# Optimization experiments

Hardware: AMD Instinct MI355X
Metric: run time of the kernel (lower is better)

Reference implementation:

```python
import jax, jax.numpy as jnp
import numpy as np

K = 20  # neighbors per point

def binq(x):
    # XNOR-Net style sign binarization with straight-through estimator
    return x + jax.lax.stop_gradient(jnp.sign(x) - x)

def knn_idx(x, k):
    # x: (B, C, N) -> (B, N, k) indices of k nearest neighbors (incl. self)
    xt = jnp.swapaxes(x, 1, 2)                      # (B, N, C)
    inner = jnp.einsum('bnc,bmc->bnm', xt, xt)
    sq = jnp.sum(xt * xt, axis=-1)                  # (B, N)
    neg_d = 2.0 * inner - sq[:, :, None] - sq[:, None, :]
    _, idx = jax.lax.top_k(neg_d, k)
    return idx

def graph_feature(x, k):
    # DGCNN edge features: (B, C, N) -> (B, 2C, N, k), plus edge index
    idx = knn_idx(x, k)
    xt = jnp.swapaxes(x, 1, 2)                      # (B, N, C)
    nb = jax.vmap(lambda t, i: t[i])(xt, idx)       # (B, N, k, C)
    ctr = jnp.broadcast_to(xt[:, :, None, :], nb.shape)
    feat = jnp.concatenate([nb - ctr, ctr], axis=-1)  # (B, N, k, 2C)
    return jnp.transpose(feat, (0, 3, 1, 2)), idx

def conv2d_block(x, W, a, s, b, p, bin_in):
    # binary-weight 1x1 conv (XNOR-Net++ channel rescale a) + eval-BN affine (s,b) + PReLU(p)
    xb = binq(x) if bin_in else x
    y = jnp.einsum('bcnk,oc->bonk', xb, binq(W))
    y = y * (a * s)[None, :, None, None] + b[None, :, None, None]
    return jnp.where(y > 0, y, p[None, :, None, None] * y)

def conv1d_block(x, W, a, s, b, p):
    y = jnp.einsum('bcn,oc->bon', binq(x), binq(W))
    y = y * (a * s)[None, :, None] + b[None, :, None]
    return jnp.where(y > 0, y, p[None, :, None] * y)

def lin_block(x, W, a, s, b, p):
    y = (binq(x) @ binq(W).T) * (a * s) + b
    return jnp.where(y > 0, y, p * y)

def forward(x0, w1, a1, s1, b1, p1, w2, a2, s2, b2, p2, w3, a3, s3, b3, p3,
            w4, a4, s4, b4, p4, w5, a5, s5, b5, p5,
            wl1, al1, sl1, bl1, pl1, wl2, al2, sl2, bl2, pl2, wl3, sl3, bl3):
    f, _ = graph_feature(x0, K)
    x1 = conv2d_block(f, w1, a1, s1, b1, p1, False).max(axis=-1)   # (B,64,N)
    f, _ = graph_feature(x1, K)
    x2 = conv2d_block(f, w2, a2, s2, b2, p2, True).max(axis=-1)    # (B,64,N)
    f, _ = graph_feature(x2, K)
    x3 = conv2d_block(f, w3, a3, s3, b3, p3, True).max(axis=-1)    # (B,128,N)
    f, _ = graph_feature(x3, K)
    x4 = conv2d_block(f, w4, a4, s4, b4, p4, True).max(axis=-1)    # (B,256,N)
    x = jnp.concatenate([x1, x2, x3, x4], axis=1)                  # (B,512,N)
    x = conv1d_block(x, w5, a5, s5, b5, p5)                        # (B,1024,N)
    x = jnp.concatenate([x.max(axis=-1), x.mean(axis=-1)], axis=1)  # (B,2048)
    x = lin_block(x, wl1, al1, sl1, bl1, pl1)                      # (B,512)
    x = lin_block(x, wl2, al2, sl2, bl2, pl2)                      # (B,256)
    return (x @ wl3.T) * sl3 + bl3                                 # (B,40) logits

def setup_inputs():
    key = jax.random.key(0)
    ks = iter(jax.random.split(key, 16))
    B, N = 16, 1024
    d = {'x0': jax.random.normal(next(ks), (B, 3, N), jnp.float32)}
    def block(name, co, ci, has_prelu=True, has_alpha=True):
        d['w' + name] = jax.random.normal(next(ks), (co, ci), jnp.float32) * 0.05
        if has_alpha:
            d['a' + name] = jnp.ones((co,), jnp.float32)
        d['s' + name] = jnp.ones((co,), jnp.float32)
        d['b' + name] = jnp.zeros((co,), jnp.float32)
        if has_prelu:
            d['p' + name] = jnp.full((co,), 0.25, jnp.float32)
    block('1', 64, 6)
    block('2', 64, 128)
    block('3', 128, 128)
    block('4', 256, 256)
    block('5', 1024, 512)
    block('l1', 512, 2048)
    block('l2', 256, 512)
    block('l3', 40, 256, has_prelu=False, has_alpha=False)
    return d

def reference(x0, w1, a1, s1, b1, p1, w2, a2, s2, b2, p2, w3, a3, s3, b3, p3,
              w4, a4, s4, b4, p4, w5, a5, s5, b5, p5,
              wl1, al1, sl1, bl1, pl1, wl2, al2, sl2, bl2, pl2, wl3, sl3, bl3):
    return forward(x0, w1, a1, s1, b1, p1, w2, a2, s2, b2, p2, w3, a3, s3, b3, p3,
                   w4, a4, s4, b4, p4, w5, a5, s5, b5, p5,
                   wl1, al1, sl1, bl1, pl1, wl2, al2, sl2, bl2, pl2, wl3, sl3, bl3)
```

## Files before the change

kernel.cpp:

```cpp
#include <hip/hip_runtime.h>
#include <math.h>

#define B 16
#define N 1024
#define KNB 20

typedef unsigned int u32;
typedef unsigned long long u64;

__device__ __forceinline__ float sgnf(float v) {
    return (v > 0.f) ? 1.f : ((v < 0.f) ? -1.f : 0.f);
}

__global__ __launch_bounds__(256) void sentinel_kernel(float* __restrict__ out, int n, float v) {
    int i = blockIdx.x * blockDim.x + threadIdx.x;
    if (i < n) out[i] = v;
}


template <int C>
__global__ __launch_bounds__(256) void sq_np_kernel(const float* __restrict__ x, int Ctot, int c0,
                                                    float* __restrict__ sq) {
    int i = blockIdx.x * blockDim.x + threadIdx.x;
    if (i >= B * N) return;
    int b = i >> 10, n = i & (N - 1);
    const float* xb = x + ((size_t)b * Ctot + c0) * N + n;
    float res;
    if (C < 8) {
        float v0 = xb[0];
        res = __fmul_rn(v0, v0);
        for (int c = 1; c < C; ++c) {
            float v = xb[(size_t)c * N];
            res = __fadd_rn(res, __fmul_rn(v, v));
        }
    } else {
        float r[8];
#pragma unroll
        for (int j = 0; j < 8; ++j) {
            float v = xb[(size_t)j * N];
            r[j] = __fmul_rn(v, v);
        }
        for (int c = 8; c < C; c += 8) {
#pragma unroll
            for (int j = 0; j < 8; ++j) {
                float v = xb[(size_t)(c + j) * N];
                r[j] = __fadd_rn(r[j], __fmul_rn(v, v));
            }
        }
        res = __fadd_rn(__fadd_rn(__fadd_rn(r[0], r[1]), __fadd_rn(r[2], r[3])),
                        __fadd_rn(__fadd_rn(r[4], r[5]), __fadd_rn(r[6], r[7])));
    }
    sq[i] = res;
}

template <int C>
__global__ __launch_bounds__(128) void knn_radix4_kernel(const float* __restrict__ x, int Ctot,
                                                         int c0, const float* __restrict__ sq,
                                                         int* __restrict__ idxout) {
    const int b = blockIdx.y;
    const int tid = threadIdx.x, wave = tid >> 6, lane = tid & 63;
    const int nbase = blockIdx.x * 8;
    __shared__ float xn[C][8];
    const float* xb = x + ((size_t)b * Ctot + c0) * N;
    for (int t = tid; t < 8 * C; t += 128) {
        int pt = t & 7, c = t >> 3;
        xn[c][pt] = xb[(size_t)c * N + nbase + pt];
    }
    __syncthreads();
    float acc[4][16];
#pragma unroll
    for (int p = 0; p < 4; ++p)
#pragma unroll
        for (int j = 0; j < 16; ++j) acc[p][j] = 0.f;
    const int w4 = wave * 4;
    for (int c = 0; c < C; ++c) {
        const float* row = xb + (size_t)c * N + lane;
        float xv0 = xn[c][w4 + 0], xv1 = xn[c][w4 + 1];
        float xv2 = xn[c][w4 + 2], xv3 = xn[c][w4 + 3];
#pragma unroll
        for (int j = 0; j < 16; ++j) {
            float rv = row[j * 64];
            acc[0][j] = __fadd_rn(acc[0][j], __fmul_rn(xv0, rv));
            acc[1][j] = __fadd_rn(acc[1][j], __fmul_rn(xv1, rv));
            acc[2][j] = __fadd_rn(acc[2][j], __fmul_rn(xv2, rv));
            acc[3][j] = __fadd_rn(acc[3][j], __fmul_rn(xv3, rv));
        }
    }
    float sqm[16];
#pragma unroll
    for (int j = 0; j < 16; ++j) sqm[j] = sq[b * N + j * 64 + lane];
    const u64 ltmask = (1ull << lane) - 1ull;
#pragma unroll
    for (int p = 0; p < 4; ++p) {
        const int n = nbase + w4 + p;
        const float sqn = sq[b * N + n];
        u32 key[16];
#pragma unroll
        for (int j = 0; j < 16; ++j) {
            float d = __fsub_rn(__fsub_rn(__fmul_rn(2.f, acc[p][j]), sqn), sqm[j]);
            u32 bits = __float_as_uint(d);
            if ((bits << 1) == 0) bits = 0;
            key[j] = (bits & 0x80000000u) ? ~bits : (bits | 0x80000000u);
        }
        u32 T = 0;
        for (int bpos = 31; bpos >= 0; --bpos) {
            u32 cand = T | (1u << bpos);
            int cnt = 0;
#pragma unroll
            for (int j = 0; j < 16; ++j) cnt += __popcll(__ballot(key[j] >= cand));
            if (cnt >= KNB) T = cand;
        }
        int* out = idxout + ((size_t)b * N + n) * KNB;
        int base = 0;
#pragma unroll
        for (int j = 0; j < 16; ++j) {
            u64 m = __ballot(key[j] > T);
            if (key[j] > T) out[base + __popcll(m & ltmask)] = j * 64 + lane;
            base += __popcll(m);
        }
        const int R = KNB - base;
        int eqb = 0;
#pragma unroll
        for (int j = 0; j < 16; ++j) {
            u64 m = __ballot(key[j] == T);
            int r = eqb + __popcll(m & ltmask);
            if (key[j] == T && r < R) out[base + r] = j * 64 + lane;
            eqb += __popcll(m);
        }
    }
}


__global__ __launch_bounds__(256) void transpose3_kernel(const float* __restrict__ x,
                                                         float* __restrict__ xT) {
    int i = blockIdx.x * blockDim.x + threadIdx.x;
    if (i >= B * N) return;
    int b = i >> 10, n = i & (N - 1);
    xT[(size_t)i * 3 + 0] = x[((size_t)b * 3 + 0) * N + n];
    xT[(size_t)i * 3 + 1] = x[((size_t)b * 3 + 1) * N + n];
    xT[(size_t)i * 3 + 2] = x[((size_t)b * 3 + 2) * N + n];
}


__global__ __launch_bounds__(256) void transpose_rm2cm_kernel(const float* __restrict__ yR, int CO,
                                                              float* __restrict__ xcat, int c0) {
    const int nb = blockIdx.x * 64, cb = blockIdx.y * 64, b = blockIdx.z;
    const int tid = threadIdx.x;
    __shared__ float t[64][65];
    for (int i = tid; i < 64 * 64; i += 256) {
        int nn = i >> 6, cc = i & 63;
        t[nn][cc] = yR[((size_t)(b * N + nb + nn)) * CO + cb + cc];
    }
    __syncthreads();
    for (int i = tid; i < 64 * 64; i += 256) {
        int cc = i >> 6, nn = i & 63;
        xcat[((size_t)b * 256 + c0 + cb + cc) * N + nb + nn] = t[nn][cc];
    }
}


template <int C, int COUT>
__global__ __launch_bounds__(COUT) void edgeconv1_kernel(
    const float* __restrict__ xR, const int* __restrict__ idx, const float* __restrict__ W,
    const float* __restrict__ aa, const float* __restrict__ ssc, const float* __restrict__ bbi,
    const float* __restrict__ pp, float* __restrict__ yR, u32* __restrict__ xss,
    u32* __restrict__ xnzs, int woff) {
    const int b = blockIdx.y, n = blockIdx.x, tid = threadIdx.x;
    __shared__ float ctr_raw[C];
    __shared__ float df[C][KNB];
    __shared__ int ids[KNB];
    const float* xb = xR + (size_t)b * N * C;
    if (tid < KNB) ids[tid] = idx[((size_t)b * N + n) * KNB + tid];
    if (tid < C) ctr_raw[tid] = xb[(size_t)n * C + tid];
    __syncthreads();
    for (int t = tid; t < C * KNB; t += COUT) {
        int c = t / KNB, k = t - c * KNB;
        df[c][k] = __fsub_rn(xb[(size_t)ids[k] * C + c], ctr_raw[c]);
    }
    __syncthreads();
    const int o = tid;
    const float* wrow = W + (size_t)o * (2 * C);
    const float as = __fmul_rn(aa[o], ssc[o]);
    const float bo = bbi[o], po = pp[o];
    float best = -3.4e38f;
    float wd[C], wc[C];
    for (int c = 0; c < C; ++c) { wd[c] = sgnf(wrow[c]); wc[c] = sgnf(wrow[C + c]); }
    for (int k = 0; k < KNB; ++k) {
        float acc = 0.f;
        for (int c = 0; c < C; ++c) acc = __fadd_rn(acc, __fmul_rn(df[c][k], wd[c]));
        for (int c = 0; c < C; ++c) acc = __fadd_rn(acc, __fmul_rn(ctr_raw[c], wc[c]));
        float y = __fadd_rn(__fmul_rn(acc, as), bo);
        y = y > 0.f ? y : __fmul_rn(po, y);
        best = fmaxf(best, y);
    }
    yR[((size_t)b * N + n) * COUT + o] = best;
    u64 bs = __ballot(best < 0.f);
    u64 bnz = __ballot(best != 0.f);
    if ((tid & 63) == 0) {
        int w = woff + (tid >> 5);
        xss[(size_t)(b * 16 + w) * N + n] = (u32)bs;
        xss[(size_t)(b * 16 + w + 1) * N + n] = (u32)(bs >> 32);
        xnzs[(size_t)(b * 16 + w) * N + n] = (u32)bnz;
        xnzs[(size_t)(b * 16 + w + 1) * N + n] = (u32)(bnz >> 32);
    }
}


__global__ __launch_bounds__(256) void pack_rows_kernel(const float* __restrict__ src, int rows,
                                                        int cols, u32* __restrict__ s,
                                                        u32* __restrict__ nz) {
    int i = blockIdx.x * blockDim.x + threadIdx.x;
    int wpr = cols >> 5;
    if (i >= rows * wpr) return;
    int r = i / wpr, w = i - r * wpr;
    const float* p = src + (size_t)r * cols + (size_t)w * 32;
    u32 sb = 0, nb = 0;
    for (int j = 0; j < 32; ++j) {
        float v = p[j];
        if (v < 0.f) sb |= (1u << j);
        if (v != 0.f) nb |= (1u << j);
    }
    s[i] = sb;
    nz[i] = nb;
}


template <int C, int COUT, bool WRITEF>
__global__ __launch_bounds__(COUT) void edgeconv_bin2_kernel(
    const float* __restrict__ xR, const int* __restrict__ idx, const u32* __restrict__ wsm,
    const u32* __restrict__ wnzm, const float* __restrict__ aa, const float* __restrict__ ssc,
    const float* __restrict__ bbi, const float* __restrict__ pp, float* __restrict__ yR,
    u32* __restrict__ xss, u32* __restrict__ xnzs, int woff) {
    constexpr int W = C / 32;
    const int b = blockIdx.y, n = blockIdx.x, tid = threadIdx.x;
    __shared__ float ctr_raw[C];
    __shared__ int ids[KNB];
    __shared__ u32 ctr_s[W], ctr_nz[W];
    __shared__ u32 dfs[KNB][W], dfnz[KNB][W];
    const float* xb = xR + (size_t)b * N * C;
    if (tid < KNB) ids[tid] = idx[((size_t)b * N + n) * KNB + tid];
    if (tid < C) {
        float v = xb[(size_t)n * C + tid];
        ctr_raw[tid] = v;
        u64 bs = __ballot(v < 0.f);
        u64 bnz = __ballot(v != 0.f);
        if ((tid & 63) == 0) {
            int wb = tid >> 5;
            ctr_s[wb] = (u32)bs;       ctr_s[wb + 1] = (u32)(bs >> 32);
            ctr_nz[wb] = (u32)bnz;     ctr_nz[wb + 1] = (u32)(bnz >> 32);
        }
    }
    __syncthreads();
    for (int t = tid; t < KNB * C; t += COUT) {
        int k = t / C, c = t - k * C;
        float v = __fsub_rn(xb[(size_t)ids[k] * C + c], ctr_raw[c]);
        u64 bs = __ballot(v < 0.f);
        u64 bnz = __ballot(v != 0.f);
        if ((c & 63) == 0) {
            int wb = c >> 5;
            dfs[k][wb] = (u32)bs;      dfs[k][wb + 1] = (u32)(bs >> 32);
            dfnz[k][wb] = (u32)bnz;    dfnz[k][wb + 1] = (u32)(bnz >> 32);
        }
    }
    __syncthreads();
    const int o = tid;
    const u32* wsrow = wsm + (size_t)o * 2 * W;
    const u32* wnzrow = wnzm + (size_t)o * 2 * W;
    u32 wds[W], wdnz[W], wcs[W], wcnz[W];
#pragma unroll
    for (int w = 0; w < W; ++w) {
        wds[w] = wsrow[w];      wcs[w] = wsrow[W + w];
        wdnz[w] = wnzrow[w];    wcnz[w] = wnzrow[W + w];
    }
    int cdot = 0;
#pragma unroll
    for (int w = 0; w < W; ++w) {
        u32 nzb = ctr_nz[w] & wcnz[w];
        u32 neg = (ctr_s[w] ^ wcs[w]) & nzb;
        cdot += __popc(nzb) - 2 * __popc(neg);
    }
    const float as = __fmul_rn(aa[o], ssc[o]);
    const float bo = bbi[o], po = pp[o];
    float best = -3.4e38f;
    for (int k = 0; k < KNB; ++k) {
        int dot = cdot;
#pragma unroll
        for (int w = 0; w < W; ++w) {
            u32 nzb = dfnz[k][w] & wdnz[w];
            u32 neg = (dfs[k][w] ^ wds[w]) & nzb;
            dot += __popc(nzb) - 2 * __popc(neg);
        }
        float y = __fadd_rn(__fmul_rn((float)dot, as), bo);
        y = y > 0.f ? y : __fmul_rn(po, y);
        best = fmaxf(best, y);
    }
    if (WRITEF) yR[((size_t)b * N + n) * COUT + o] = best;
    u64 bs = __ballot(best < 0.f);
    u64 bnz = __ballot(best != 0.f);
    if ((tid & 63) == 0) {
        int w = woff + (tid >> 5);
        xss[(size_t)(b * 16 + w) * N + n] = (u32)bs;
        xss[(size_t)(b * 16 + w + 1) * N + n] = (u32)(bs >> 32);
        xnzs[(size_t)(b * 16 + w) * N + n] = (u32)bnz;
        xnzs[(size_t)(b * 16 + w + 1) * N + n] = (u32)(bnz >> 32);
    }
}


__global__ __launch_bounds__(256) void conv1d_bin_pool_kernel(
    const u32* __restrict__ xs, const u32* __restrict__ xnz, const u32* __restrict__ w5s,
    const u32* __restrict__ w5nz, const float* __restrict__ aa, const float* __restrict__ ssc,
    const float* __restrict__ bbi, const float* __restrict__ pp, float* __restrict__ pmax,
    float* __restrict__ psum) {
    const int b = blockIdx.y;
    const int otile = blockIdx.x & 3;
    const int nq = blockIdx.x >> 2;
    const int tid = threadIdx.x;
    const int o = otile * 256 + tid;
    __shared__ u32 shs[64][21];
    __shared__ u32 shnz[64][21];
    u32 ws[16], wnz[16];
#pragma unroll
    for (int w = 0; w < 16; ++w) {
        ws[w] = w5s[(size_t)o * 16 + w];
        wnz[w] = w5nz[(size_t)o * 16 + w];
    }
    const int nbase = nq * 64;
    for (int t = tid; t < 16 * 64; t += 256) {
        int w = t >> 6, nl = t & 63;
        shs[nl][w] = xs[((size_t)b * 16 + w) * N + nbase + nl];
        shnz[nl][w] = xnz[((size_t)b * 16 + w) * N + nbase + nl];
    }
    __syncthreads();
    const float as = __fmul_rn(aa[o], ssc[o]);
    const float bo = bbi[o], po = pp[o];
    float m = -3.4e38f, sum = 0.f;
    for (int nl = 0; nl < 64; ++nl) {
        int dot = 0;
#pragma unroll
        for (int w = 0; w < 16; ++w) {
            u32 nzb = shnz[nl][w] & wnz[w];
            u32 neg = (shs[nl][w] ^ ws[w]) & nzb;
            dot += __popc(nzb) - 2 * __popc(neg);
        }
        float y = __fadd_rn(__fmul_rn((float)dot, as), bo);
        y = y > 0.f ? y : __fmul_rn(po, y);
        m = fmaxf(m, y);
        sum = __fadd_rn(sum, y);
    }
    pmax[((size_t)b * 1024 + o) * 16 + nq] = m;
    psum[((size_t)b * 1024 + o) * 16 + nq] = sum;
}

__global__ __launch_bounds__(256) void pool_reduce_kernel(const float* __restrict__ pmax,
                                                          const float* __restrict__ psum,
                                                          float* __restrict__ pooled) {
    int i = blockIdx.x * blockDim.x + threadIdx.x;
    if (i >= B * 1024) return;
    int b = i >> 10, o = i & 1023;
    const float* pm = pmax + (size_t)i * 16;
    const float* ps = psum + (size_t)i * 16;
    float m = -3.4e38f, s = 0.f;
    for (int t = 0; t < 16; ++t) { m = fmaxf(m, pm[t]); s = __fadd_rn(s, ps[t]); }
    pooled[(size_t)b * 2048 + o] = m;
    pooled[(size_t)b * 2048 + 1024 + o] = __fmul_rn(s, (1.f / 1024.f));
}

__global__ __launch_bounds__(256) void pack_pooled_kernel(const float* __restrict__ pooled,
                                                          u32* __restrict__ s,
                                                          u32* __restrict__ nz) {
    int i = blockIdx.x * blockDim.x + threadIdx.x;
    if (i >= B * 64) return;
    const float* p = pooled + (size_t)i * 32;
    u32 sb = 0, nb = 0;
    for (int j = 0; j < 32; ++j) {
        float v = p[j];
        if (v < 0.f) sb |= (1u << j);
        if (v != 0.f) nb |= (1u << j);
    }
    s[i] = sb;
    nz[i] = nb;
}


__global__ __launch_bounds__(256) void lin1_bin_kernel(
    const u32* __restrict__ xs, const u32* __restrict__ xnz, const u32* __restrict__ wls,
    const u32* __restrict__ wlnz, const float* __restrict__ aa, const float* __restrict__ ssc,
    const float* __restrict__ bbi, const float* __restrict__ pp, u32* __restrict__ l1s,
    u32* __restrict__ l1nz) {
    const int b = blockIdx.y, otile = blockIdx.x, tid = threadIdx.x;
    const int o = otile * 256 + tid;
    __shared__ u32 sxs[64], sxnz[64];
    if (tid < 64) { sxs[tid] = xs[b * 64 + tid]; sxnz[tid] = xnz[b * 64 + tid]; }
    __syncthreads();
    const u32* wsr = wls + (size_t)o * 64;
    const u32* wnzr = wlnz + (size_t)o * 64;
    int dot = 0;
#pragma unroll
    for (int w = 0; w < 64; ++w) {
        u32 nzb = sxnz[w] & wnzr[w];
        u32 neg = (sxs[w] ^ wsr[w]) & nzb;
        dot += __popc(nzb) - 2 * __popc(neg);
    }
    float y = __fadd_rn(__fmul_rn((float)dot, __fmul_rn(aa[o], ssc[o])), bbi[o]);
    y = y > 0.f ? y : __fmul_rn(pp[o], y);
    u64 bs = __ballot(y < 0.f);
    u64 bnz = __ballot(y != 0.f);
    if ((tid & 63) == 0) {
        int w = otile * 8 + (tid >> 5);
        l1s[b * 16 + w] = (u32)bs;       l1s[b * 16 + w + 1] = (u32)(bs >> 32);
        l1nz[b * 16 + w] = (u32)bnz;     l1nz[b * 16 + w + 1] = (u32)(bnz >> 32);
    }
}

__global__ __launch_bounds__(256) void lin2_bin_kernel(
    const u32* __restrict__ xs, const u32* __restrict__ xnz, const u32* __restrict__ wls,
    const u32* __restrict__ wlnz, const float* __restrict__ aa, const float* __restrict__ ssc,
    const float* __restrict__ bbi, const float* __restrict__ pp, float* __restrict__ out) {
    const int b = blockIdx.x, o = threadIdx.x;
    __shared__ u32 sxs[16], sxnz[16];
    if (o < 16) { sxs[o] = xs[b * 16 + o]; sxnz[o] = xnz[b * 16 + o]; }
    __syncthreads();
    const u32* wsr = wls + (size_t)o * 16;
    const u32* wnzr = wlnz + (size_t)o * 16;
    int dot = 0;
#pragma unroll
    for (int w = 0; w < 16; ++w) {
        u32 nzb = sxnz[w] & wnzr[w];
        u32 neg = (sxs[w] ^ wsr[w]) & nzb;
        dot += __popc(nzb) - 2 * __popc(neg);
    }
    float y = __fadd_rn(__fmul_rn((float)dot, __fmul_rn(aa[o], ssc[o])), bbi[o]);
    out[b * 256 + o] = y > 0.f ? y : __fmul_rn(pp[o], y);
}

__global__ __launch_bounds__(64) void lin3_kernel(const float* __restrict__ xin,
                                                  const float* __restrict__ W,
                                                  const float* __restrict__ ssc,
                                                  const float* __restrict__ bbi,
                                                  float* __restrict__ out) {
    int b = blockIdx.x, j = threadIdx.x;
    if (j >= 40) return;
    const float* wrow = W + j * 256;
    const float* xb = xin + b * 256;
    double acc = 0.0;
    for (int c = 0; c < 256; ++c) acc = fma((double)xb[c], (double)wrow[c], acc);
    out[b * 40 + j] = __fadd_rn(__fmul_rn((float)acc, ssc[j]), bbi[j]);
}

extern "C" void kernel_launch(void* const* d_in, const int* in_sizes, int n_in, void* d_out,
                              int out_size, void* d_ws, size_t ws_size, hipStream_t stream) {
    float* outp = (float*)d_out;
    auto sentinel = [&](float code) {
        sentinel_kernel<<<(640 + 255) / 256, 256, 0, stream>>>(outp, 640, code * 1.0e6f);
    };
    if (n_in != 39) { sentinel(1.f); return; }
    static const int expect[39] = {
        16 * 3 * 1024,
        64 * 6, 64, 64, 64, 64,
        64 * 128, 64, 64, 64, 64,
        128 * 128, 128, 128, 128, 128,
        256 * 256, 256, 256, 256, 256,
        1024 * 512, 1024, 1024, 1024, 1024,
        512 * 2048, 512, 512, 512, 512,
        256 * 512, 256, 256, 256, 256,
        40 * 256, 40, 40
    };
    for (int i = 0; i < 39; ++i)
        if (in_sizes[i] != expect[i]) { sentinel(2.f); return; }
    if (out_size != 640) { sentinel(3.f); return; }

    const float* x0 = (const float*)d_in[0];
    const float *w1 = (const float*)d_in[1], *a1 = (const float*)d_in[2],
                *s1 = (const float*)d_in[3], *b1 = (const float*)d_in[4],
                *p1 = (const float*)d_in[5];
    const float *a2 = (const float*)d_in[7], *s2 = (const float*)d_in[8],
                *b2 = (const float*)d_in[9], *p2 = (const float*)d_in[10];
    const float *a3 = (const float*)d_in[12], *s3 = (const float*)d_in[13],
                *b3 = (const float*)d_in[14], *p3 = (const float*)d_in[15];
    const float *a4 = (const float*)d_in[17], *s4 = (const float*)d_in[18],
                *b4 = (const float*)d_in[19], *p4 = (const float*)d_in[20];
    const float *a5 = (const float*)d_in[22], *s5 = (const float*)d_in[23],
                *b5 = (const float*)d_in[24], *p5 = (const float*)d_in[25];
    const float *w2 = (const float*)d_in[6], *w3 = (const float*)d_in[11],
                *w4 = (const float*)d_in[16], *w5 = (const float*)d_in[21];
    const float *wl1 = (const float*)d_in[26], *al1 = (const float*)d_in[27],
                *sl1 = (const float*)d_in[28], *bl1 = (const float*)d_in[29],
                *pl1 = (const float*)d_in[30];
    const float *wl2 = (const float*)d_in[31], *al2 = (const float*)d_in[32],
                *sl2 = (const float*)d_in[33], *bl2 = (const float*)d_in[34],
                *pl2 = (const float*)d_in[35];
    const float *wl3 = (const float*)d_in[36], *sl3 = (const float*)d_in[37],
                *bl3 = (const float*)d_in[38];

    char* ws = (char*)d_ws;
    size_t off = 0;
    auto alloc = [&](size_t bytes) -> void* {
        void* p = ws + off;
        off += (bytes + 255) & ~(size_t)255;
        return p;
    };
    float* xcat = (float*)alloc((size_t)B * 256 * N * 4);
    float* yA = (float*)alloc((size_t)B * N * 128 * 4);
    float* yB = (float*)alloc((size_t)B * N * 64 * 4);
    float* x0R = (float*)alloc((size_t)B * N * 3 * 4);
    int* idxb = (int*)alloc((size_t)B * N * KNB * 4);
    float* sqb = (float*)alloc((size_t)B * N * 4);
    u32* w2s_ = (u32*)alloc(64 * 4 * 4);     u32* w2nz_ = (u32*)alloc(64 * 4 * 4);
    u32* w3s_ = (u32*)alloc(128 * 4 * 4);    u32* w3nz_ = (u32*)alloc(128 * 4 * 4);
    u32* w4s_ = (u32*)alloc(256 * 8 * 4);    u32* w4nz_ = (u32*)alloc(256 * 8 * 4);
    u32* w5s_ = (u32*)alloc(1024 * 16 * 4);  u32* w5nz_ = (u32*)alloc(1024 * 16 * 4);
    u32* wl1s_ = (u32*)alloc(512 * 64 * 4);  u32* wl1nz_ = (u32*)alloc(512 * 64 * 4);
    u32* wl2s_ = (u32*)alloc(256 * 16 * 4);  u32* wl2nz_ = (u32*)alloc(256 * 16 * 4);
    u32* xss = (u32*)alloc((size_t)B * 16 * N * 4);
    u32* xnzs = (u32*)alloc((size_t)B * 16 * N * 4);
    u32* pls = (u32*)alloc((size_t)B * 64 * 4);
    u32* plnz = (u32*)alloc((size_t)B * 64 * 4);
    u32* l1s = (u32*)alloc((size_t)B * 16 * 4);
    u32* l1nz = (u32*)alloc((size_t)B * 16 * 4);
    float* pmax = (float*)alloc((size_t)B * 1024 * 16 * 4);
    float* psum = (float*)alloc((size_t)B * 1024 * 16 * 4);
    float* pooled = (float*)alloc((size_t)B * 2048 * 4);
    float* l2o = (float*)alloc((size_t)B * 256 * 4);
    if (off > ws_size) { sentinel(4.f); return; }

    pack_rows_kernel<<<1, 256, 0, stream>>>(w2, 64, 128, w2s_, w2nz_);
    pack_rows_kernel<<<2, 256, 0, stream>>>(w3, 128, 128, w3s_, w3nz_);
    pack_rows_kernel<<<8, 256, 0, stream>>>(w4, 256, 256, w4s_, w4nz_);
    pack_rows_kernel<<<64, 256, 0, stream>>>(w5, 1024, 512, w5s_, w5nz_);
    pack_rows_kernel<<<128, 256, 0, stream>>>(wl1, 512, 2048, wl1s_, wl1nz_);
    pack_rows_kernel<<<16, 256, 0, stream>>>(wl2, 256, 512, wl2s_, wl2nz_);

    dim3 gnb(N, B);
    dim3 gknn(N / 8, B);
    const int npt = (B * N + 255) / 256;
    sq_np_kernel<3><<<npt, 256, 0, stream>>>(x0, 3, 0, sqb);
    transpose3_kernel<<<npt, 256, 0, stream>>>(x0, x0R);
    knn_radix4_kernel<3><<<gknn, 128, 0, stream>>>(x0, 3, 0, sqb, idxb);
    edgeconv1_kernel<3, 64>
        <<<gnb, 64, 0, stream>>>(x0R, idxb, w1, a1, s1, b1, p1, yA, xss, xnzs, 0);
    transpose_rm2cm_kernel<<<dim3(16, 1, B), 256, 0, stream>>>(yA, 64, xcat, 0);
    sq_np_kernel<64><<<npt, 256, 0, stream>>>(xcat, 256, 0, sqb);
    knn_radix4_kernel<64><<<gknn, 128, 0, stream>>>(xcat, 256, 0, sqb, idxb);
    edgeconv_bin2_kernel<64, 64, true>
        <<<gnb, 64, 0, stream>>>(yA, idxb, w2s_, w2nz_, a2, s2, b2, p2, yB, xss, xnzs, 2);
    transpose_rm2cm_kernel<<<dim3(16, 1, B), 256, 0, stream>>>(yB, 64, xcat, 64);
    sq_np_kernel<64><<<npt, 256, 0, stream>>>(xcat, 256, 64, sqb);
    knn_radix4_kernel<64><<<gknn, 128, 0, stream>>>(xcat, 256, 64, sqb, idxb);
    edgeconv_bin2_kernel<64, 128, true>
        <<<gnb, 128, 0, stream>>>(yB, idxb, w3s_, w3nz_, a3, s3, b3, p3, yA, xss, xnzs, 4);
    transpose_rm2cm_kernel<<<dim3(16, 2, B), 256, 0, stream>>>(yA, 128, xcat, 128);
    sq_np_kernel<128><<<npt, 256, 0, stream>>>(xcat, 256, 128, sqb);
    knn_radix4_kernel<128><<<gknn, 128, 0, stream>>>(xcat, 256, 128, sqb, idxb);
    edgeconv_bin2_kernel<128, 256, false>
        <<<gnb, 256, 0, stream>>>(yA, idxb, w4s_, w4nz_, a4, s4, b4, p4, nullptr, xss, xnzs, 8);
    conv1d_bin_pool_kernel<<<dim3(64, B), 256, 0, stream>>>(xss, xnzs, w5s_, w5nz_, a5, s5, b5,
                                                            p5, pmax, psum);
    pool_reduce_kernel<<<(B * 1024 + 255) / 256, 256, 0, stream>>>(pmax, psum, pooled);
    pack_pooled_kernel<<<(B * 64 + 255) / 256, 256, 0, stream>>>(pooled, pls, plnz);
    lin1_bin_kernel<<<dim3(2, B), 256, 0, stream>>>(pls, plnz, wl1s_, wl1nz_, al1, sl1, bl1, pl1,
                                                    l1s, l1nz);
    lin2_bin_kernel<<<B, 256, 0, stream>>>(l1s, l1nz, wl2s_, wl2nz_, al2, sl2, bl2, pl2, l2o);
    lin3_kernel<<<B, 64, 0, stream>>>(l2o, wl3, sl3, bl3, outp);
}
```

Measured before the change: 627.9 us.

## Halve points per kNN block, vectorize row loads, and raise occupancy bound

```diff
diff --git a/kernel.cpp b/kernel.cpp
--- a/kernel.cpp
+++ b/kernel.cpp
@@ -54,45 +54,50 @@
 }
 
 template <int C>
-__global__ __launch_bounds__(128) void knn_radix4_kernel(const float* __restrict__ x, int Ctot,
-                                                         int c0, const float* __restrict__ sq,
-                                                         int* __restrict__ idxout) {
+__global__ __launch_bounds__(128, 8) void knn_radix4_kernel(const float* __restrict__ x, int Ctot,
+                                                            int c0, const float* __restrict__ sq,
+                                                            int* __restrict__ idxout) {
     const int b = blockIdx.y;
     const int tid = threadIdx.x, wave = tid >> 6, lane = tid & 63;
-    const int nbase = blockIdx.x * 8;
-    __shared__ float xn[C][8];
+    const int nbase = blockIdx.x * 4;
+    __shared__ float xn[C][4];
     const float* xb = x + ((size_t)b * Ctot + c0) * N;
-    for (int t = tid; t < 8 * C; t += 128) {
-        int pt = t & 7, c = t >> 3;
+    for (int t = tid; t < 4 * C; t += 128) {
+        int pt = t & 3, c = t >> 2;
         xn[c][pt] = xb[(size_t)c * N + nbase + pt];
     }
     __syncthreads();
-    float acc[4][16];
-#pragma unroll
-    for (int p = 0; p < 4; ++p)
+    float acc[2][16];
+#pragma unroll
+    for (int p = 0; p < 2; ++p)
 #pragma unroll
         for (int j = 0; j < 16; ++j) acc[p][j] = 0.f;
-    const int w4 = wave * 4;
+    const int w2p = wave * 2;
     for (int c = 0; c < C; ++c) {
-        const float* row = xb + (size_t)c * N + lane;
-        float xv0 = xn[c][w4 + 0], xv1 = xn[c][w4 + 1];
-        float xv2 = xn[c][w4 + 2], xv3 = xn[c][w4 + 3];
+        const float4* rp4 = reinterpret_cast<const float4*>(xb + (size_t)c * N + lane * 16);
+        float4 r0 = rp4[0], r1 = rp4[1], r2 = rp4[2], r3 = rp4[3];
+        float rv[16] = {r0.x, r0.y, r0.z, r0.w, r1.x, r1.y, r1.z, r1.w,
+                        r2.x, r2.y, r2.z, r2.w, r3.x, r3.y, r3.z, r3.w};
+        float xv0 = xn[c][w2p + 0], xv1 = xn[c][w2p + 1];
 #pragma unroll
         for (int j = 0; j < 16; ++j) {
-            float rv = row[j * 64];
-            acc[0][j] = __fadd_rn(acc[0][j], __fmul_rn(xv0, rv));
-            acc[1][j] = __fadd_rn(acc[1][j], __fmul_rn(xv1, rv));
-            acc[2][j] = __fadd_rn(acc[2][j], __fmul_rn(xv2, rv));
-            acc[3][j] = __fadd_rn(acc[3][j], __fmul_rn(xv3, rv));
+            acc[0][j] = __fadd_rn(acc[0][j], __fmul_rn(xv0, rv[j]));
+            acc[1][j] = __fadd_rn(acc[1][j], __fmul_rn(xv1, rv[j]));
         }
     }
     float sqm[16];
-#pragma unroll
-    for (int j = 0; j < 16; ++j) sqm[j] = sq[b * N + j * 64 + lane];
+    {
+        const float4* sp4 = reinterpret_cast<const float4*>(sq + b * N + lane * 16);
+        float4 s0 = sp4[0], s1 = sp4[1], s2 = sp4[2], s3 = sp4[3];
+        sqm[0] = s0.x;  sqm[1] = s0.y;  sqm[2] = s0.z;  sqm[3] = s0.w;
+        sqm[4] = s1.x;  sqm[5] = s1.y;  sqm[6] = s1.z;  sqm[7] = s1.w;
+        sqm[8] = s2.x;  sqm[9] = s2.y;  sqm[10] = s2.z; sqm[11] = s2.w;
+        sqm[12] = s3.x; sqm[13] = s3.y; sqm[14] = s3.z; sqm[15] = s3.w;
+    }
     const u64 ltmask = (1ull << lane) - 1ull;
 #pragma unroll
-    for (int p = 0; p < 4; ++p) {
-        const int n = nbase + w4 + p;
+    for (int p = 0; p < 2; ++p) {
+        const int n = nbase + w2p + p;
         const float sqn = sq[b * N + n];
         u32 key[16];
 #pragma unroll
@@ -115,17 +120,25 @@
 #pragma unroll
         for (int j = 0; j < 16; ++j) {
             u64 m = __ballot(key[j] > T);
-            if (key[j] > T) out[base + __popcll(m & ltmask)] = j * 64 + lane;
+            if (key[j] > T) out[base + __popcll(m & ltmask)] = lane * 16 + j;
             base += __popcll(m);
         }
         const int R = KNB - base;
-        int eqb = 0;
+        int s_lt = 0;
+        u64 e[16];
 #pragma unroll
         for (int j = 0; j < 16; ++j) {
-            u64 m = __ballot(key[j] == T);
-            int r = eqb + __popcll(m & ltmask);
-            if (key[j] == T && r < R) out[base + r] = j * 64 + lane;
-            eqb += __popcll(m);
+            e[j] = __ballot(key[j] == T);
+            s_lt += __popcll(e[j] & ltmask);
+        }
+        int ownp = 0;
+#pragma unroll
+        for (int j = 0; j < 16; ++j) {
+            if (key[j] == T) {
+                int r = s_lt + ownp;
+                if (r < R) out[base + r] = lane * 16 + j;
+                ownp++;
+            }
         }
     }
 }
@@ -532,7 +545,7 @@
     pack_rows_kernel<<<16, 256, 0, stream>>>(wl2, 256, 512, wl2s_, wl2nz_);
 
     dim3 gnb(N, B);
-    dim3 gknn(N / 8, B);
+    dim3 gknn(N / 4, B);
     const int npt = (B * N + 255) / 256;
     sq_np_kernel<3><<<npt, 256, 0, stream>>>(x0, 3, 0, sqb);
     transpose3_kernel<<<npt, 256, 0, stream>>>(x0, x0R);
```

Measured after the change: 1.120 ms. 78.3% more time.
